# Kernel optimization log

Measured on AMD Instinct MI355X. Metric: run time of the kernel, lower is better.

Reference implementation:

```python
import jax, jax.numpy as jnp
import numpy as np

N = 100000
E = 1000000
H = 128
DF = 64
TOTAL_GENES = 20000
NUM_PERTS = 5000


def setup_inputs() -> dict:
    key = jax.random.key(0)
    ks = jax.random.split(key, 32)
    d_in1 = DF + H  # all_feat=True: concat raw feats with gene embedding

    def g(k, shape, scale=0.05):
        return jax.random.normal(k, shape, dtype=jnp.float32) * scale

    inp = {
        'x': jax.random.normal(ks[0], (N, DF), dtype=jnp.float32),
        'edge_index': jax.random.randint(ks[1], (2, E), 0, N),
        'edge_attr': jax.random.normal(ks[2], (E, 1), dtype=jnp.float32),
        'pert': jax.random.randint(ks[3], (N,), 0, NUM_PERTS),
        'ctrl': jax.random.normal(ks[4], (N, 1), dtype=jnp.float32),
        'pos': jax.random.randint(ks[5], (N,), 0, TOTAL_GENES),
        # learned parameters
        'gene_table': g(ks[6], (TOTAL_GENES, H), 1.0),
        'pert_table': g(ks[7], (NUM_PERTS, H), 1.0),
        'W1': g(ks[8], (d_in1, H)), 'a_src1': g(ks[9], (H,)), 'a_dst1': g(ks[10], (H,)), 'b1': g(ks[11], (H,)),
        'Wl1': g(ks[12], (d_in1, H)), 'bl1': g(ks[13], (H,)),
        'W2': g(ks[14], (H, H)), 'a_src2': g(ks[15], (H,)), 'a_dst2': g(ks[16], (H,)), 'b2': g(ks[17], (H,)),
        'Wl2': g(ks[18], (H, H)), 'bl2': g(ks[19], (H,)),
        'Wm1': g(ks[20], (2 * H + 1, H // 2)), 'bm1': g(ks[21], (H // 2,)),
        'Wm2': g(ks[22], (H // 2, 1)), 'bm2': g(ks[23], (1,)),
    }
    return inp


def gat_conv(x, src, dst, W, a_src, a_dst, b, n_nodes):
    # PyG GATConv, heads=1, concat=False, negative_slope=0.2, add_self_loops
    h = x @ W                         # [N, H]
    asrc = h @ a_src                  # [N]
    adst = h @ a_dst                  # [N]
    loop = jnp.arange(n_nodes)
    s = jnp.concatenate([src, loop])  # [E+N]
    d = jnp.concatenate([dst, loop])
    e = jax.nn.leaky_relu(asrc[s] + adst[d], negative_slope=0.2)
    m = jax.ops.segment_max(e, d, num_segments=n_nodes)
    ex = jnp.exp(e - m[d])
    denom = jax.ops.segment_sum(ex, d, num_segments=n_nodes)
    alpha = ex / (denom[d] + 1e-16)
    out = jax.ops.segment_sum(h[s] * alpha[:, None], d, num_segments=n_nodes)
    return out + b


def _forward(x, edge_attr, ctrl, gene_table, pert_table,
             W1, a_src1, a_dst1, b1, Wl1, bl1,
             W2, a_src2, a_dst2, b2, Wl2, bl2,
             Wm1, bm1, Wm2, bm2,
             edge_index, pert, pos):
    src, dst = edge_index[0], edge_index[1]
    # gene embedding with max_norm=True (rows renormed to norm <= 1.0)
    pe = gene_table[pos]
    nrm = jnp.linalg.norm(pe, axis=-1, keepdims=True)
    pe = jnp.where(nrm > 1.0, pe / (nrm + 1e-7), pe)
    h = jnp.concatenate([x, pe], axis=1)            # [N, DF+H]
    h = gat_conv(h, src, dst, W1, a_src1, a_dst1, b1, x.shape[0]) + h @ Wl1 + bl1
    h = jax.nn.relu(h)
    h = gat_conv(h, src, dst, W2, a_src2, a_dst2, b2, x.shape[0]) + h @ Wl2 + bl2
    z = jnp.concatenate([h, ctrl, pert_table[pert]], axis=1)  # [N, 2H+1]
    z = jax.nn.relu(z @ Wm1 + bm1)
    z = jax.nn.relu(z @ Wm2 + bm2)
    return z.squeeze(1)


def reference(x, edge_index, edge_attr, pert, ctrl, pos,
              gene_table, pert_table,
              W1, a_src1, a_dst1, b1, Wl1, bl1,
              W2, a_src2, a_dst2, b2, Wl2, bl2,
              Wm1, bm1, Wm2, bm2):
    return _forward(x, edge_attr, ctrl, gene_table, pert_table,
                    W1, a_src1, a_dst1, b1, Wl1, bl1,
                    W2, a_src2, a_dst2, b2, Wl2, bl2,
                    Wm1, bm1, Wm2, bm2,
                    edge_index, pert, pos)
```

## Files before the change

### kernel.cpp

```cpp
#include <hip/hip_runtime.h>
#include <hip/hip_bf16.h>

typedef __bf16 bf16;
typedef __bf16 bf16x8 __attribute__((ext_vector_type(8)));
typedef __bf16 bf16x4 __attribute__((ext_vector_type(4)));
typedef __bf16 bf16x2 __attribute__((ext_vector_type(2)));
typedef float f32x4 __attribute__((ext_vector_type(4)));

#define CAP 48

__device__ __forceinline__ float b2f(bf16 v) { return (float)v; }
__device__ __forceinline__ bf16 f2b(float v) { return (bf16)v; }

__device__ __forceinline__ float leaky(float x) { return fmaxf(x, 0.2f * x); }

__device__ __forceinline__ bf16x8 zero8() {
    bf16x8 v;
    #pragma unroll
    for (int j = 0; j < 8; ++j) v[j] = (bf16)0.0f;
    return v;
}

__device__ __forceinline__ void swizzle_one(const float* __restrict__ W, bf16* __restrict__ dst,
                                            int f, int NT, int Kreal, int C) {
    int kb = f / (NT * 64);
    int rem = f % (NT * 64);
    int nt = rem / 64;
    int ln = rem % 64;
    int q = ln >> 4, m = ln & 15;
    int c = nt * 16 + m;
    bf16x8 v;
    #pragma unroll
    for (int j = 0; j < 8; ++j) {
        int k = kb * 32 + q * 8 + j;
        v[j] = (k < Kreal) ? f2b(W[k * C + c]) : (bf16)0.0f;
    }
    *reinterpret_cast<bf16x8*>(dst + f * 8) = v;
}

__global__ void h0_prep_kernel(const float* __restrict__ x,
                               const float* __restrict__ gene_table,
                               const int* __restrict__ pos,
                               bf16* __restrict__ h0, int n,
                               const float* __restrict__ W1, const float* __restrict__ Wl1,
                               const float* __restrict__ W2, const float* __restrict__ Wl2,
                               const float* __restrict__ Wm1,
                               bf16* __restrict__ w1s, bf16* __restrict__ wl1s,
                               bf16* __restrict__ w2s, bf16* __restrict__ wl2s,
                               bf16* __restrict__ wm1s,
                               const int* __restrict__ e_src, const int* __restrict__ e_dst,
                               int* __restrict__ cnt, int* __restrict__ colidx,
                               int e, int nbsc, int nboth) {
    int g5 = blockIdx.x / 5, r5 = blockIdx.x % 5;
    if (r5 == 0) {
        if (g5 >= nbsc) return;
        int i = g5 * blockDim.x + threadIdx.x;
        if (i < e) {
            int d = __builtin_nontemporal_load(e_dst + i);
            int s = __builtin_nontemporal_load(e_src + i);
            int k = atomicAdd(&cnt[d], 1);
            if (k < CAP) __builtin_nontemporal_store(s, colidx + d * CAP + k);
        }
        return;
    }
    int ob = g5 * 4 + (r5 - 1);
    if (ob >= nboth) return;
    if (ob < 49) {
        int g = ob * blockDim.x + threadIdx.x;
        if (g < 3072)        swizzle_one(W1,  w1s,  g,          8, 192, 128);
        else if (g < 6144)   swizzle_one(Wl1, wl1s, g - 3072,   8, 192, 128);
        else if (g < 8192)   swizzle_one(W2,  w2s,  g - 6144,   8, 128, 128);
        else if (g < 10240)  swizzle_one(Wl2, wl2s, g - 8192,   8, 128, 128);
        else if (g < 12544)  swizzle_one(Wm1, wm1s, g - 10240,  4, 257,  64);
        return;
    }
    int wid = (ob - 49) * 8 + (threadIdx.x >> 5);
    int l = threadIdx.x & 31;
    if (wid >= n) return;
    const float* g = gene_table + (long long)pos[wid] * 128;
    float4 p = reinterpret_cast<const float4*>(g)[l];
    float ss = p.x * p.x + p.y * p.y + p.z * p.z + p.w * p.w;
    #pragma unroll
    for (int o = 16; o; o >>= 1) ss += __shfl_xor(ss, o);
    float nrm = sqrtf(ss);
    float sc = nrm > 1.0f ? 1.0f / (nrm + 1e-7f) : 1.0f;
    bf16* orow = h0 + (long long)wid * 192;
    float2 xv = reinterpret_cast<const float2*>(x + (long long)wid * 64)[l];
    bf16x2 xb; xb[0] = f2b(xv.x); xb[1] = f2b(xv.y);
    *reinterpret_cast<bf16x2*>(orow + 2 * l) = xb;
    bf16x4 gb;
    gb[0] = f2b(p.x * sc); gb[1] = f2b(p.y * sc);
    gb[2] = f2b(p.z * sc); gb[3] = f2b(p.w * sc);
    *reinterpret_cast<bf16x4*>(orow + 64 + 4 * l) = gb;
}

template <int KB>
__global__ __launch_bounds__(256) void gemm_dual_kernel(
    const bf16* __restrict__ A, int lda,
    const bf16* __restrict__ Wg, const bf16* __restrict__ Wl,
    const float* __restrict__ bias_l,
    bf16* __restrict__ outg, bf16* __restrict__ outl, int ldo, int nrows,
    const float* __restrict__ attn_s, const float* __restrict__ attn_d,
    float* __restrict__ asrc, float* __restrict__ adst) {
    const int NTT = 8;
    __shared__ float sA[64][2];
    int tid = threadIdx.x;
    int wave = tid >> 6, lane = tid & 63;
    int q = lane >> 4, m = lane & 15;
    int nt0 = (wave & 1) * 4;
    long long row_base = (long long)blockIdx.x * 64 + (wave >> 1) * 32;
    long long r0 = row_base + m;
    long long r1 = row_base + 16 + m;
    bool v0 = r0 < nrows, v1 = r1 < nrows;

    f32x4 accg[2][4], accl[2][4];
    #pragma unroll
    for (int t = 0; t < 2; ++t)
        #pragma unroll
        for (int nt = 0; nt < 4; ++nt) {
            f32x4 z = {0.f, 0.f, 0.f, 0.f};
            accg[t][nt] = z; accl[t][nt] = z;
        }

    bf16x8 b0 = v0 ? *reinterpret_cast<const bf16x8*>(A + r0 * lda + q * 8) : zero8();
    bf16x8 b1 = v1 ? *reinterpret_cast<const bf16x8*>(A + r1 * lda + q * 8) : zero8();
    #pragma unroll
    for (int kb = 0; kb < KB; ++kb) {
        bf16x8 nb0, nb1;
        if (kb + 1 < KB) {
            nb0 = v0 ? *reinterpret_cast<const bf16x8*>(A + r0 * lda + (kb + 1) * 32 + q * 8) : zero8();
            nb1 = v1 ? *reinterpret_cast<const bf16x8*>(A + r1 * lda + (kb + 1) * 32 + q * 8) : zero8();
        }
        #pragma unroll
        for (int nt = 0; nt < 4; ++nt) {
            bf16x8 wg = *reinterpret_cast<const bf16x8*>(Wg + ((kb * NTT + nt0 + nt) * 64 + lane) * 8);
            bf16x8 wl = *reinterpret_cast<const bf16x8*>(Wl + ((kb * NTT + nt0 + nt) * 64 + lane) * 8);
            accg[0][nt] = __builtin_amdgcn_mfma_f32_16x16x32_bf16(wg, b0, accg[0][nt], 0, 0, 0);
            accg[1][nt] = __builtin_amdgcn_mfma_f32_16x16x32_bf16(wg, b1, accg[1][nt], 0, 0, 0);
            accl[0][nt] = __builtin_amdgcn_mfma_f32_16x16x32_bf16(wl, b0, accl[0][nt], 0, 0, 0);
            accl[1][nt] = __builtin_amdgcn_mfma_f32_16x16x32_bf16(wl, b1, accl[1][nt], 0, 0, 0);
        }
        b0 = nb0; b1 = nb1;
    }
    #pragma unroll
    for (int t = 0; t < 2; ++t) {
        long long row = t ? r1 : r0;
        if (row < nrows) {
            #pragma unroll
            for (int nt = 0; nt < 4; ++nt) {
                int c0 = (nt0 + nt) * 16 + q * 4;
                bf16x4 og, ol;
                #pragma unroll
                for (int r = 0; r < 4; ++r) {
                    og[r] = f2b(accg[t][nt][r]);
                    ol[r] = f2b(accl[t][nt][r] + bias_l[c0 + r]);
                }
                *reinterpret_cast<bf16x4*>(outg + row * ldo + c0) = og;
                *reinterpret_cast<bf16x4*>(outl + row * ldo + c0) = ol;
            }
        }
    }
    float svt[2], dvt[2];
    #pragma unroll
    for (int t = 0; t < 2; ++t) {
        float sv = 0.f, dv = 0.f;
        #pragma unroll
        for (int nt = 0; nt < 4; ++nt) {
            int c0 = (nt0 + nt) * 16 + q * 4;
            #pragma unroll
            for (int r = 0; r < 4; ++r) {
                float v = accg[t][nt][r];
                sv = fmaf(v, attn_s[c0 + r], sv);
                dv = fmaf(v, attn_d[c0 + r], dv);
            }
        }
        sv += __shfl_xor(sv, 16); sv += __shfl_xor(sv, 32);
        dv += __shfl_xor(dv, 16); dv += __shfl_xor(dv, 32);
        svt[t] = sv; dvt[t] = dv;
        if ((wave & 1) == 0 && q == 0) {
            int rloc = (wave >> 1) * 32 + t * 16 + m;
            sA[rloc][0] = sv; sA[rloc][1] = dv;
        }
    }
    __syncthreads();
    #pragma unroll
    for (int t = 0; t < 2; ++t) {
        long long row = t ? r1 : r0;
        if ((wave & 1) == 1 && q == 0 && row < nrows) {
            int rloc = (wave >> 1) * 32 + t * 16 + m;
            asrc[row] = svt[t] + sA[rloc][0];
            adst[row] = dvt[t] + sA[rloc][1];
        }
    }
}

template <int KB, int NT>
__global__ __launch_bounds__(256) void gemm_mlp_kernel(
    const bf16* __restrict__ A, int lda,
    const bf16* __restrict__ Wsw,
    const float* __restrict__ bias, int nrows,
    const float* __restrict__ Wm2, const float* __restrict__ bm2,
    float* __restrict__ out_final) {
    int tid = threadIdx.x;
    int wave = tid >> 6, lane = tid & 63;
    int q = lane >> 4, m = lane & 15;
    long long row_base = (long long)blockIdx.x * 128 + wave * 32;
    long long r0 = row_base + m;
    long long r1 = row_base + 16 + m;
    bool v0 = r0 < nrows, v1 = r1 < nrows;

    f32x4 acc[2][NT];
    #pragma unroll
    for (int t = 0; t < 2; ++t)
        #pragma unroll
        for (int nt = 0; nt < NT; ++nt) {
            f32x4 z = {0.f, 0.f, 0.f, 0.f};
            acc[t][nt] = z;
        }

    bf16x8 b0 = v0 ? *reinterpret_cast<const bf16x8*>(A + r0 * lda + q * 8) : zero8();
    bf16x8 b1 = v1 ? *reinterpret_cast<const bf16x8*>(A + r1 * lda + q * 8) : zero8();
    #pragma unroll
    for (int kb = 0; kb < KB; ++kb) {
        bf16x8 nb0, nb1;
        if (kb + 1 < KB) {
            nb0 = v0 ? *reinterpret_cast<const bf16x8*>(A + r0 * lda + (kb + 1) * 32 + q * 8) : zero8();
            nb1 = v1 ? *reinterpret_cast<const bf16x8*>(A + r1 * lda + (kb + 1) * 32 + q * 8) : zero8();
        }
        #pragma unroll
        for (int nt = 0; nt < NT; ++nt) {
            bf16x8 w = *reinterpret_cast<const bf16x8*>(Wsw + ((kb * NT + nt) * 64 + lane) * 8);
            acc[0][nt] = __builtin_amdgcn_mfma_f32_16x16x32_bf16(w, b0, acc[0][nt], 0, 0, 0);
            acc[1][nt] = __builtin_amdgcn_mfma_f32_16x16x32_bf16(w, b1, acc[1][nt], 0, 0, 0);
        }
        b0 = nb0; b1 = nb1;
    }
    #pragma unroll
    for (int t = 0; t < 2; ++t) {
        float sv = 0.f;
        #pragma unroll
        for (int nt = 0; nt < NT; ++nt) {
            int c0 = nt * 16 + q * 4;
            #pragma unroll
            for (int r = 0; r < 4; ++r) {
                float v = fmaxf(acc[t][nt][r] + bias[c0 + r], 0.0f);
                sv = fmaf(v, Wm2[c0 + r], sv);
            }
        }
        sv += __shfl_xor(sv, 16); sv += __shfl_xor(sv, 32);
        long long row = t ? r1 : r0;
        if (q == 0 && row < nrows) out_final[row] = fmaxf(sv + bm2[0], 0.0f);
    }
}

__global__ void gat_edge_kernel(const int* __restrict__ cnt, const int* __restrict__ colidx,
                                const float* __restrict__ asrc, const float* __restrict__ adst,
                                const bf16* __restrict__ hgat, const bf16* __restrict__ hlin,
                                const float* __restrict__ b_gat, int relu,
                                bf16* __restrict__ out, int ldo, int n,
                                const float* __restrict__ ctrl,
                                const float* __restrict__ pert_table,
                                const int* __restrict__ pert) {
    int d = blockIdx.x * 8 + (threadIdx.x >> 5);
    int lane = threadIdx.x & 31;
    if (d >= n) return;
    float ad = adst[d];
    float e_self = leaky(asrc[d] + ad);
    int cn = cnt[d]; if (cn > CAP) cn = CAP;
    bool val0 = lane < cn;
    bool val1 = lane + 32 < cn;
    int sj0 = val0 ? colidx[d * CAP + lane] : d;
    int sj1 = val1 ? colidx[d * CAP + 32 + lane] : d;
    float ej0 = val0 ? leaky(asrc[sj0] + ad) : -1e30f;
    float ej1 = val1 ? leaky(asrc[sj1] + ad) : -1e30f;
    float mx = fmaxf(ej0, ej1);
    #pragma unroll
    for (int o = 16; o; o >>= 1) mx = fmaxf(mx, __shfl_xor(mx, o, 32));
    mx = fmaxf(mx, e_self);
    float wj0 = val0 ? __expf(ej0 - mx) : 0.0f;
    float wj1 = val1 ? __expf(ej1 - mx) : 0.0f;
    float ws = __expf(e_self - mx);
    float sm = wj0 + wj1;
    #pragma unroll
    for (int o = 16; o; o >>= 1) sm += __shfl_xor(sm, o, 32);
    float den = sm + ws;
    bf16x4 hl = *reinterpret_cast<const bf16x4*>(hlin + (long long)d * 128 + 4 * lane);
    float4 bg = *reinterpret_cast<const float4*>(b_gat + 4 * lane);
    bf16x4 hd = *reinterpret_cast<const bf16x4*>(hgat + (long long)d * 128 + 4 * lane);
    float acc0 = ws * b2f(hd[0]), acc1 = ws * b2f(hd[1]);
    float acc2 = ws * b2f(hd[2]), acc3 = ws * b2f(hd[3]);
    int c1 = cn < 32 ? cn : 32;
    for (int j = 0; j < c1; j += 4) {
        int s0 = __shfl(sj0, j, 32), s1 = __shfl(sj0, j + 1, 32);
        int s2 = __shfl(sj0, j + 2, 32), s3 = __shfl(sj0, j + 3, 32);
        float w0 = __shfl(wj0, j, 32), w1 = __shfl(wj0, j + 1, 32);
        float w2 = __shfl(wj0, j + 2, 32), w3 = __shfl(wj0, j + 3, 32);
        bf16x4 h0v = *reinterpret_cast<const bf16x4*>(hgat + (long long)s0 * 128 + 4 * lane);
        bf16x4 h1v = *reinterpret_cast<const bf16x4*>(hgat + (long long)s1 * 128 + 4 * lane);
        bf16x4 h2v = *reinterpret_cast<const bf16x4*>(hgat + (long long)s2 * 128 + 4 * lane);
        bf16x4 h3v = *reinterpret_cast<const bf16x4*>(hgat + (long long)s3 * 128 + 4 * lane);
        acc0 = fmaf(w0, b2f(h0v[0]), acc0); acc1 = fmaf(w0, b2f(h0v[1]), acc1);
        acc2 = fmaf(w0, b2f(h0v[2]), acc2); acc3 = fmaf(w0, b2f(h0v[3]), acc3);
        acc0 = fmaf(w1, b2f(h1v[0]), acc0); acc1 = fmaf(w1, b2f(h1v[1]), acc1);
        acc2 = fmaf(w1, b2f(h1v[2]), acc2); acc3 = fmaf(w1, b2f(h1v[3]), acc3);
        acc0 = fmaf(w2, b2f(h2v[0]), acc0); acc1 = fmaf(w2, b2f(h2v[1]), acc1);
        acc2 = fmaf(w2, b2f(h2v[2]), acc2); acc3 = fmaf(w2, b2f(h2v[3]), acc3);
        acc0 = fmaf(w3, b2f(h3v[0]), acc0); acc1 = fmaf(w3, b2f(h3v[1]), acc1);
        acc2 = fmaf(w3, b2f(h3v[2]), acc2); acc3 = fmaf(w3, b2f(h3v[3]), acc3);
    }
    for (int j = 32; j < cn; j += 4) {
        int s0 = __shfl(sj1, j - 32, 32), s1 = __shfl(sj1, j - 31, 32);
        int s2 = __shfl(sj1, j - 30, 32), s3 = __shfl(sj1, j - 29, 32);
        float w0 = __shfl(wj1, j - 32, 32), w1 = __shfl(wj1, j - 31, 32);
        float w2 = __shfl(wj1, j - 30, 32), w3 = __shfl(wj1, j - 29, 32);
        bf16x4 h0v = *reinterpret_cast<const bf16x4*>(hgat + (long long)s0 * 128 + 4 * lane);
        bf16x4 h1v = *reinterpret_cast<const bf16x4*>(hgat + (long long)s1 * 128 + 4 * lane);
        bf16x4 h2v = *reinterpret_cast<const bf16x4*>(hgat + (long long)s2 * 128 + 4 * lane);
        bf16x4 h3v = *reinterpret_cast<const bf16x4*>(hgat + (long long)s3 * 128 + 4 * lane);
        acc0 = fmaf(w0, b2f(h0v[0]), acc0); acc1 = fmaf(w0, b2f(h0v[1]), acc1);
        acc2 = fmaf(w0, b2f(h0v[2]), acc2); acc3 = fmaf(w0, b2f(h0v[3]), acc3);
        acc0 = fmaf(w1, b2f(h1v[0]), acc0); acc1 = fmaf(w1, b2f(h1v[1]), acc1);
        acc2 = fmaf(w1, b2f(h1v[2]), acc2); acc3 = fmaf(w1, b2f(h1v[3]), acc3);
        acc0 = fmaf(w2, b2f(h2v[0]), acc0); acc1 = fmaf(w2, b2f(h2v[1]), acc1);
        acc2 = fmaf(w2, b2f(h2v[2]), acc2); acc3 = fmaf(w2, b2f(h2v[3]), acc3);
        acc0 = fmaf(w3, b2f(h3v[0]), acc0); acc1 = fmaf(w3, b2f(h3v[1]), acc1);
        acc2 = fmaf(w3, b2f(h3v[2]), acc2); acc3 = fmaf(w3, b2f(h3v[3]), acc3);
    }
    float inv = 1.0f / den;
    float o0 = acc0 * inv + bg.x + b2f(hl[0]);
    float o1 = acc1 * inv + bg.y + b2f(hl[1]);
    float o2 = acc2 * inv + bg.z + b2f(hl[2]);
    float o3 = acc3 * inv + bg.w + b2f(hl[3]);
    if (relu) {
        o0 = fmaxf(o0, 0.0f); o1 = fmaxf(o1, 0.0f);
        o2 = fmaxf(o2, 0.0f); o3 = fmaxf(o3, 0.0f);
    }
    bf16* orow = out + (long long)d * ldo;
    bf16x4 ov; ov[0] = f2b(o0); ov[1] = f2b(o1); ov[2] = f2b(o2); ov[3] = f2b(o3);
    *reinterpret_cast<bf16x4*>(orow + 4 * lane) = ov;
    if (pert) {
        const float* p = pert_table + (long long)pert[d] * 128;
        if (lane == 0) orow[128] = f2b(ctrl[d]);
        orow[129 + lane] = f2b(p[lane]);
        orow[161 + lane] = f2b(p[32 + lane]);
        orow[193 + lane] = f2b(p[64 + lane]);
        orow[225 + lane] = f2b(p[96 + lane]);
        if (lane < 31) orow[257 + lane] = (bf16)0.0f;
    }
}

extern "C" void kernel_launch(void* const* d_in, const int* in_sizes, int n_in,
                              void* d_out, int out_size, void* d_ws, size_t ws_size,
                              hipStream_t stream) {
    const int N = in_sizes[0] / 64;
    const int E = in_sizes[1] / 2;

    const float* x          = (const float*)d_in[0];
    const int*   ei         = (const int*)d_in[1];
    const int*   e_src      = ei;
    const int*   e_dst      = ei + E;
    const int*   pert       = (const int*)d_in[3];
    const float* ctrl       = (const float*)d_in[4];
    const int*   pos        = (const int*)d_in[5];
    const float* gene_table = (const float*)d_in[6];
    const float* pert_table = (const float*)d_in[7];
    const float* W1   = (const float*)d_in[8];
    const float* a_s1 = (const float*)d_in[9];
    const float* a_d1 = (const float*)d_in[10];
    const float* b1   = (const float*)d_in[11];
    const float* Wl1  = (const float*)d_in[12];
    const float* bl1  = (const float*)d_in[13];
    const float* W2   = (const float*)d_in[14];
    const float* a_s2 = (const float*)d_in[15];
    const float* a_d2 = (const float*)d_in[16];
    const float* b2   = (const float*)d_in[17];
    const float* Wl2  = (const float*)d_in[18];
    const float* bl2  = (const float*)d_in[19];
    const float* Wm1  = (const float*)d_in[20];
    const float* bm1  = (const float*)d_in[21];
    const float* Wm2  = (const float*)d_in[22];
    const float* bm2  = (const float*)d_in[23];

    char* ws = (char*)d_ws;
    size_t off = 0;
    auto alloc = [&](size_t bytes) {
        char* p = ws + off;
        off = (off + bytes + 255) & ~(size_t)255;
        return p;
    };
    bf16* hgat   = (bf16*)alloc((size_t)N * 128 * 2);
    bf16* hlin   = (bf16*)alloc((size_t)N * 128 * 2);
    bf16* h0     = (bf16*)alloc((size_t)N * 192 * 2);
    bf16* h1     = (bf16*)alloc((size_t)N * 128 * 2);
    bf16* zbuf   = h0;
    float* asrc  = (float*)alloc((size_t)N * 4);
    float* adst  = (float*)alloc((size_t)N * 4);
    int* cnt     = (int*)alloc((size_t)N * 4);
    int* colidx  = (int*)alloc((size_t)N * CAP * 4);
    bf16* w1s    = (bf16*)alloc((size_t)3072 * 8 * 2);
    bf16* wl1s   = (bf16*)alloc((size_t)3072 * 8 * 2);
    bf16* w2s    = (bf16*)alloc((size_t)2048 * 8 * 2);
    bf16* wl2s   = (bf16*)alloc((size_t)2048 * 8 * 2);
    bf16* wm1s   = (bf16*)alloc((size_t)2304 * 8 * 2);
    (void)ws_size; (void)n_in; (void)out_size;

    float* out = (float*)d_out;

    const int NBH8 = (N + 7) / 8;
    const int NBOTH = 49 + NBH8;
    const int NBSC = (E + 255) / 256;
    const int NG5 = (NBSC > (NBOTH + 3) / 4) ? NBSC : (NBOTH + 3) / 4;
    const int NBFUSED = NG5 * 5;
    const int NBG64 = (N + 63) / 64;
    const int NBG128 = (N + 127) / 128;
    dim3 blk(256);
    dim3 gridWave((N + 7) / 8);

    hipMemsetAsync(cnt, 0, (size_t)N * 4, stream);
    hipLaunchKernelGGL(h0_prep_kernel, dim3(NBFUSED), blk, 0, stream,
                       x, gene_table, pos, h0, N,
                       W1, Wl1, W2, Wl2, Wm1, w1s, wl1s, w2s, wl2s, wm1s,
                       e_src, e_dst, cnt, colidx, E, NBSC, NBOTH);
    hipLaunchKernelGGL((gemm_dual_kernel<6>), dim3(NBG64), blk, 0, stream,
                       h0, 192, w1s, wl1s, bl1, hgat, hlin, 128, N,
                       a_s1, a_d1, asrc, adst);
    hipLaunchKernelGGL(gat_edge_kernel, gridWave, blk, 0, stream,
                       cnt, colidx, asrc, adst, hgat, hlin, b1, 1, h1, 128, N,
                       (const float*)nullptr, (const float*)nullptr, (const int*)nullptr);
    hipLaunchKernelGGL((gemm_dual_kernel<4>), dim3(NBG64), blk, 0, stream,
                       h1, 128, w2s, wl2s, bl2, hgat, hlin, 128, N,
                       a_s2, a_d2, asrc, adst);
    hipLaunchKernelGGL(gat_edge_kernel, gridWave, blk, 0, stream,
                       cnt, colidx, asrc, adst, hgat, hlin, b2, 0, zbuf, 288, N,
                       ctrl, pert_table, pert);
    hipLaunchKernelGGL((gemm_mlp_kernel<9, 4>), dim3(NBG128), blk, 0, stream,
                       zbuf, 288, wm1s, bm1, N, Wm2, bm2, out);
}
```

Measured before the change: 378.7 us.

## Fuse gene-embedding prep into layer-1 GEMM via shared-memory staging

The embedding gather, max-norm renormalization and concatenation with x now happen inside the first dual GEMM. Each block stages the bf16 rows in shared memory instead of writing an intermediate h0 buffer to global memory and reading it back. The prep kernel shrinks to edge scatter plus weight swizzling. This removes about 38 MB of global round-trip traffic, at the cost of 25 KB of LDS per block, which may lower GEMM occupancy. The staging stores are scalar bf16 writes with possible bank conflicts.

Measured after the change: 428.1 us. 1.13x slower.

```diff
diff --git a/kernel.cpp b/kernel.cpp
--- a/kernel.cpp
+++ b/kernel.cpp
@@ -38,35 +38,17 @@
     *reinterpret_cast<bf16x8*>(dst + f * 8) = v;
 }
 
-__global__ void h0_prep_kernel(const float* __restrict__ x,
-                               const float* __restrict__ gene_table,
-                               const int* __restrict__ pos,
-                               bf16* __restrict__ h0, int n,
+__global__ void scatter_kernel(const int* __restrict__ e_src, const int* __restrict__ e_dst,
+                               int* __restrict__ cnt, int* __restrict__ colidx, int e,
                                const float* __restrict__ W1, const float* __restrict__ Wl1,
                                const float* __restrict__ W2, const float* __restrict__ Wl2,
                                const float* __restrict__ Wm1,
                                bf16* __restrict__ w1s, bf16* __restrict__ wl1s,
                                bf16* __restrict__ w2s, bf16* __restrict__ wl2s,
-                               bf16* __restrict__ wm1s,
-                               const int* __restrict__ e_src, const int* __restrict__ e_dst,
-                               int* __restrict__ cnt, int* __restrict__ colidx,
-                               int e, int nbsc, int nboth) {
-    int g5 = blockIdx.x / 5, r5 = blockIdx.x % 5;
-    if (r5 == 0) {
-        if (g5 >= nbsc) return;
-        int i = g5 * blockDim.x + threadIdx.x;
-        if (i < e) {
-            int d = __builtin_nontemporal_load(e_dst + i);
-            int s = __builtin_nontemporal_load(e_src + i);
-            int k = atomicAdd(&cnt[d], 1);
-            if (k < CAP) __builtin_nontemporal_store(s, colidx + d * CAP + k);
-        }
-        return;
-    }
-    int ob = g5 * 4 + (r5 - 1);
-    if (ob >= nboth) return;
-    if (ob < 49) {
-        int g = ob * blockDim.x + threadIdx.x;
+                               bf16* __restrict__ wm1s) {
+    int bid = blockIdx.x;
+    if (bid < 49) {
+        int g = bid * blockDim.x + threadIdx.x;
         if (g < 3072)        swizzle_one(W1,  w1s,  g,          8, 192, 128);
         else if (g < 6144)   swizzle_one(Wl1, wl1s, g - 3072,   8, 192, 128);
         else if (g < 8192)   swizzle_one(W2,  w2s,  g - 6144,   8, 128, 128);
@@ -74,24 +56,144 @@
         else if (g < 12544)  swizzle_one(Wm1, wm1s, g - 10240,  4, 257,  64);
         return;
     }
-    int wid = (ob - 49) * 8 + (threadIdx.x >> 5);
-    int l = threadIdx.x & 31;
-    if (wid >= n) return;
-    const float* g = gene_table + (long long)pos[wid] * 128;
-    float4 p = reinterpret_cast<const float4*>(g)[l];
-    float ss = p.x * p.x + p.y * p.y + p.z * p.z + p.w * p.w;
-    #pragma unroll
-    for (int o = 16; o; o >>= 1) ss += __shfl_xor(ss, o);
-    float nrm = sqrtf(ss);
-    float sc = nrm > 1.0f ? 1.0f / (nrm + 1e-7f) : 1.0f;
-    bf16* orow = h0 + (long long)wid * 192;
-    float2 xv = reinterpret_cast<const float2*>(x + (long long)wid * 64)[l];
-    bf16x2 xb; xb[0] = f2b(xv.x); xb[1] = f2b(xv.y);
-    *reinterpret_cast<bf16x2*>(orow + 2 * l) = xb;
-    bf16x4 gb;
-    gb[0] = f2b(p.x * sc); gb[1] = f2b(p.y * sc);
-    gb[2] = f2b(p.z * sc); gb[3] = f2b(p.w * sc);
-    *reinterpret_cast<bf16x4*>(orow + 64 + 4 * l) = gb;
+    int i = (bid - 49) * blockDim.x + threadIdx.x;
+    if (i < e) {
+        int d = __builtin_nontemporal_load(e_dst + i);
+        int s = __builtin_nontemporal_load(e_src + i);
+        int k = atomicAdd(&cnt[d], 1);
+        if (k < CAP) __builtin_nontemporal_store(s, colidx + d * CAP + k);
+    }
+}
+
+template <int KB>
+__global__ __launch_bounds__(256) void gemm_l1_kernel(
+    const float* __restrict__ x,
+    const float* __restrict__ gene_table,
+    const int* __restrict__ pos,
+    const bf16* __restrict__ Wg, const bf16* __restrict__ Wl,
+    const float* __restrict__ bias_l,
+    bf16* __restrict__ outg, bf16* __restrict__ outl, int ldo, int nrows,
+    const float* __restrict__ attn_s, const float* __restrict__ attn_d,
+    float* __restrict__ asrc, float* __restrict__ adst) {
+    const int NTT = 8;
+    __shared__ bf16 sH[64][200];
+    __shared__ float sA[64][2];
+    int tid = threadIdx.x;
+
+    {
+        int rsub = tid >> 5, l32 = tid & 31;
+        #pragma unroll
+        for (int rr = 0; rr < 8; ++rr) {
+            int rloc = rr * 8 + rsub;
+            long long row = (long long)blockIdx.x * 64 + rloc;
+            if (row < nrows) {
+                const float* g = gene_table + (long long)pos[row] * 128;
+                float4 p = reinterpret_cast<const float4*>(g)[l32];
+                float ss = p.x * p.x + p.y * p.y + p.z * p.z + p.w * p.w;
+                #pragma unroll
+                for (int o = 16; o; o >>= 1) ss += __shfl_xor(ss, o, 32);
+                float nrm = sqrtf(ss);
+                float sc = nrm > 1.0f ? 1.0f / (nrm + 1e-7f) : 1.0f;
+                float2 xv = reinterpret_cast<const float2*>(x + row * 64)[l32];
+                sH[rloc][2 * l32]     = f2b(xv.x);
+                sH[rloc][2 * l32 + 1] = f2b(xv.y);
+                sH[rloc][64 + 4 * l32 + 0] = f2b(p.x * sc);
+                sH[rloc][64 + 4 * l32 + 1] = f2b(p.y * sc);
+                sH[rloc][64 + 4 * l32 + 2] = f2b(p.z * sc);
+                sH[rloc][64 + 4 * l32 + 3] = f2b(p.w * sc);
+            } else {
+                sH[rloc][2 * l32]     = (bf16)0.0f;
+                sH[rloc][2 * l32 + 1] = (bf16)0.0f;
+                sH[rloc][64 + 4 * l32 + 0] = (bf16)0.0f;
+                sH[rloc][64 + 4 * l32 + 1] = (bf16)0.0f;
+                sH[rloc][64 + 4 * l32 + 2] = (bf16)0.0f;
+                sH[rloc][64 + 4 * l32 + 3] = (bf16)0.0f;
+            }
+        }
+    }
+    __syncthreads();
+
+    int wave = tid >> 6, lane = tid & 63;
+    int q = lane >> 4, m = lane & 15;
+    int nt0 = (wave & 1) * 4;
+    int r0loc = (wave >> 1) * 32 + m;
+    long long row_base = (long long)blockIdx.x * 64 + (wave >> 1) * 32;
+    long long r0 = row_base + m;
+    long long r1 = row_base + 16 + m;
+
+    f32x4 accg[2][4], accl[2][4];
+    #pragma unroll
+    for (int t = 0; t < 2; ++t)
+        #pragma unroll
+        for (int nt = 0; nt < 4; ++nt) {
+            f32x4 z = {0.f, 0.f, 0.f, 0.f};
+            accg[t][nt] = z; accl[t][nt] = z;
+        }
+
+    #pragma unroll
+    for (int kb = 0; kb < KB; ++kb) {
+        bf16x8 b0 = *reinterpret_cast<const bf16x8*>(&sH[r0loc][kb * 32 + q * 8]);
+        bf16x8 b1 = *reinterpret_cast<const bf16x8*>(&sH[r0loc + 16][kb * 32 + q * 8]);
+        #pragma unroll
+        for (int nt = 0; nt < 4; ++nt) {
+            bf16x8 wg = *reinterpret_cast<const bf16x8*>(Wg + ((kb * NTT + nt0 + nt) * 64 + lane) * 8);
+            bf16x8 wl = *reinterpret_cast<const bf16x8*>(Wl + ((kb * NTT + nt0 + nt) * 64 + lane) * 8);
+            accg[0][nt] = __builtin_amdgcn_mfma_f32_16x16x32_bf16(wg, b0, accg[0][nt], 0, 0, 0);
+            accg[1][nt] = __builtin_amdgcn_mfma_f32_16x16x32_bf16(wg, b1, accg[1][nt], 0, 0, 0);
+            accl[0][nt] = __builtin_amdgcn_mfma_f32_16x16x32_bf16(wl, b0, accl[0][nt], 0, 0, 0);
+            accl[1][nt] = __builtin_amdgcn_mfma_f32_16x16x32_bf16(wl, b1, accl[1][nt], 0, 0, 0);
+        }
+    }
+    #pragma unroll
+    for (int t = 0; t < 2; ++t) {
+        long long row = t ? r1 : r0;
+        if (row < nrows) {
+            #pragma unroll
+            for (int nt = 0; nt < 4; ++nt) {
+                int c0 = (nt0 + nt) * 16 + q * 4;
+                bf16x4 og, ol;
+                #pragma unroll
+                for (int r = 0; r < 4; ++r) {
+                    og[r] = f2b(accg[t][nt][r]);
+                    ol[r] = f2b(accl[t][nt][r] + bias_l[c0 + r]);
+                }
+                *reinterpret_cast<bf16x4*>(outg + row * ldo + c0) = og;
+                *reinterpret_cast<bf16x4*>(outl + row * ldo + c0) = ol;
+            }
+        }
+    }
+    float svt[2], dvt[2];
+    #pragma unroll
+    for (int t = 0; t < 2; ++t) {
+        float sv = 0.f, dv = 0.f;
+        #pragma unroll
+        for (int nt = 0; nt < 4; ++nt) {
+            int c0 = (nt0 + nt) * 16 + q * 4;
+            #pragma unroll
+            for (int r = 0; r < 4; ++r) {
+                float v = accg[t][nt][r];
+                sv = fmaf(v, attn_s[c0 + r], sv);
+                dv = fmaf(v, attn_d[c0 + r], dv);
+            }
+        }
+        sv += __shfl_xor(sv, 16); sv += __shfl_xor(sv, 32);
+        dv += __shfl_xor(dv, 16); dv += __shfl_xor(dv, 32);
+        svt[t] = sv; dvt[t] = dv;
+        if ((wave & 1) == 0 && q == 0) {
+            int rloc = (wave >> 1) * 32 + t * 16 + m;
+            sA[rloc][0] = sv; sA[rloc][1] = dv;
+        }
+    }
+    __syncthreads();
+    #pragma unroll
+    for (int t = 0; t < 2; ++t) {
+        long long row = t ? r1 : r0;
+        if ((wave & 1) == 1 && q == 0 && row < nrows) {
+            int rloc = (wave >> 1) * 32 + t * 16 + m;
+            asrc[row] = svt[t] + sA[rloc][0];
+            adst[row] = dvt[t] + sA[rloc][1];
+        }
+    }
 }
 
 template <int KB>
@@ -390,9 +492,9 @@
     };
     bf16* hgat   = (bf16*)alloc((size_t)N * 128 * 2);
     bf16* hlin   = (bf16*)alloc((size_t)N * 128 * 2);
-    bf16* h0     = (bf16*)alloc((size_t)N * 192 * 2);
+    bf16* zregion= (bf16*)alloc((size_t)N * 192 * 2);
     bf16* h1     = (bf16*)alloc((size_t)N * 128 * 2);
-    bf16* zbuf   = h0;
+    bf16* zbuf   = zregion;
     float* asrc  = (float*)alloc((size_t)N * 4);
     float* adst  = (float*)alloc((size_t)N * 4);
     int* cnt     = (int*)alloc((size_t)N * 4);
@@ -406,23 +508,18 @@
 
     float* out = (float*)d_out;
 
-    const int NBH8 = (N + 7) / 8;
-    const int NBOTH = 49 + NBH8;
     const int NBSC = (E + 255) / 256;
-    const int NG5 = (NBSC > (NBOTH + 3) / 4) ? NBSC : (NBOTH + 3) / 4;
-    const int NBFUSED = NG5 * 5;
     const int NBG64 = (N + 63) / 64;
     const int NBG128 = (N + 127) / 128;
     dim3 blk(256);
     dim3 gridWave((N + 7) / 8);
 
     hipMemsetAsync(cnt, 0, (size_t)N * 4, stream);
-    hipLaunchKernelGGL(h0_prep_kernel, dim3(NBFUSED), blk, 0, stream,
-                       x, gene_table, pos, h0, N,
-                       W1, Wl1, W2, Wl2, Wm1, w1s, wl1s, w2s, wl2s, wm1s,
-                       e_src, e_dst, cnt, colidx, E, NBSC, NBOTH);
-    hipLaunchKernelGGL((gemm_dual_kernel<6>), dim3(NBG64), blk, 0, stream,
-                       h0, 192, w1s, wl1s, bl1, hgat, hlin, 128, N,
+    hipLaunchKernelGGL(scatter_kernel, dim3(49 + NBSC), blk, 0, stream,
+                       e_src, e_dst, cnt, colidx, E,
+                       W1, Wl1, W2, Wl2, Wm1, w1s, wl1s, w2s, wl2s, wm1s);
+    hipLaunchKernelGGL((gemm_l1_kernel<6>), dim3(NBG64), blk, 0, stream,
+                       x, gene_table, pos, w1s, wl1s, bl1, hgat, hlin, 128, N,
                        a_s1, a_d1, asrc, adst);
     hipLaunchKernelGGL(gat_edge_kernel, gridWave, blk, 0, stream,
                        cnt, colidx, asrc, adst, hgat, hlin, b1, 1, h1, 128, N,
```
